# Performance work log

Hardware: AMD Instinct MI355X
Metric: run time of the kernel (lower is better)

Reference implementation:

```python
import jax, jax.numpy as jnp
import numpy as np

KEEP_RATIO = 0.1
FS = 8          # feature_size
BN_EPS = 1e-5


def dct_matrix(N):
    # Orthonormal DCT-II matrix: D[k,n] = s_k * cos(pi*(2n+1)*k/(2N))
    n = jnp.arange(N, dtype=jnp.float32)
    k = n[:, None]
    D = jnp.cos(jnp.pi * (2.0 * n + 1.0) * k / (2.0 * N))
    scale = jnp.full((N, 1), jnp.sqrt(2.0 / N), jnp.float32).at[0, 0].set(jnp.sqrt(1.0 / N))
    return D * scale


def bilinear_resize(x, out_h, out_w):
    # torch F.interpolate bilinear, align_corners=False (half-pixel centers, no antialias)
    def coords(in_size, out):
        src = (jnp.arange(out, dtype=jnp.float32) + 0.5) * (in_size / out) - 0.5
        src = jnp.clip(src, 0.0, in_size - 1.0)
        i0 = jnp.floor(src).astype(jnp.int32)
        i1 = jnp.minimum(i0 + 1, in_size - 1)
        return i0, i1, src - i0.astype(jnp.float32)
    r0, r1, rw = coords(x.shape[2], out_h)
    c0, c1, cw = coords(x.shape[3], out_w)
    x = x[:, :, r0, :] * (1.0 - rw)[:, None] + x[:, :, r1, :] * rw[:, None]
    x = x[:, :, :, c0] * (1.0 - cw) + x[:, :, :, c1] * cw
    return x


def apply_dct(x):
    H, W = x.shape[2], x.shape[3]
    Dh, Dw = dct_matrix(H), dct_matrix(W)
    # 2D DCT-II (ortho): Y = Dh @ X @ Dw^T
    y = jnp.einsum('hi,bcij,wj->bchw', Dh, x, Dw)
    hk, wk = int(H * KEEP_RATIO), int(W * KEEP_RATIO)
    mask = jnp.zeros((H, W), x.dtype).at[:hk, :wk].set(1.0)  # low-pass keep top-left block
    y = y * mask
    # inverse DCT (ortho): X = Dh^T @ Y @ Dw
    x = jnp.einsum('ih,bchw,jw->bcij', Dh, y, Dw)
    return bilinear_resize(x, FS, FS)


def generate_gradient_image(x):
    # scipy convolve2d flips the kernel, but flipped sobel == -sobel and we take abs,
    # so plain correlation with sobel is equivalent. boundary='wrap' -> circular pad.
    sx = jnp.array([[-1, 0, 1], [-2, 0, 2], [-1, 0, 1]], jnp.float32)
    sy = jnp.array([[-1, -2, -1], [0, 0, 0], [1, 2, 1]], jnp.float32)
    kern = jnp.stack([sx, sy])[:, None]  # [2,1,3,3]
    B, C, H, W = x.shape
    xc = x.reshape(B * C, 1, H, W)
    xp = jnp.pad(xc, ((0, 0), (0, 0), (1, 1), (1, 1)), mode='wrap')
    g = jax.lax.conv_general_dilated(xp, kern, (1, 1), 'VALID')  # [B*C,2,H,W]
    grad = jnp.sqrt(g[:, 0] ** 2 + g[:, 1] ** 2).reshape(B, C, H, W)
    return bilinear_resize(grad, FS, FS)


def feature_extractor(x, w, b, gamma, beta):
    y = jax.lax.conv_general_dilated(x, w, (1, 1), ((1, 1), (1, 1)))
    y = y + b[None, :, None, None]
    # BatchNorm (inference: running_mean=0, running_var=1)
    y = y * (gamma / jnp.sqrt(1.0 + BN_EPS))[None, :, None, None] + beta[None, :, None, None]
    y = jax.nn.relu(y)
    # input is already FS x FS, so AdaptiveAvgPool2d((8,8)) is the identity
    return y


def setup_inputs() -> dict:
    key = jax.random.key(0)
    ks = jax.random.split(key, 10)
    B, C, H, W = 128, 3, 256, 256
    return {
        'x': jax.random.normal(ks[0], (B, C, H, W), jnp.float32),
        'conv_dct_w': jax.random.normal(ks[1], (64, 3, 3, 3), jnp.float32) * 0.1,
        'conv_dct_b': jnp.zeros((64,), jnp.float32),
        'bn_dct_g': jnp.ones((64,), jnp.float32),
        'bn_dct_b': jnp.zeros((64,), jnp.float32),
        'conv_grad_w': jax.random.normal(ks[2], (64, 3, 3, 3), jnp.float32) * 0.1,
        'conv_grad_b': jnp.zeros((64,), jnp.float32),
        'bn_grad_g': jnp.ones((64,), jnp.float32),
        'bn_grad_b': jnp.zeros((64,), jnp.float32),
        'fus_w': jax.random.normal(ks[3], (1, 64), jnp.float32) * 0.1,
        'fus_b': jnp.zeros((1,), jnp.float32),
        'cls_w': jax.random.normal(ks[4], (2, 64 * FS * FS), jnp.float32) * 0.02,
        'cls_b': jnp.zeros((2,), jnp.float32),
    }


def reference(x, conv_dct_w, conv_dct_b, bn_dct_g, bn_dct_b,
              conv_grad_w, conv_grad_b, bn_grad_g, bn_grad_b,
              fus_w, fus_b, cls_w, cls_b):
    dct_in = apply_dct(x)                       # [B,3,8,8]
    grad_in = generate_gradient_image(x)        # [B,3,8,8]
    d = feature_extractor(dct_in, conv_dct_w, conv_dct_b, bn_dct_g, bn_dct_b)    # [B,64,8,8]
    g = feature_extractor(grad_in, conv_grad_w, conv_grad_b, bn_grad_g, bn_grad_b)
    # FeatureFusion: weight = sigmoid(fc(avgpool(d+g)))
    s = jnp.mean(d + g, axis=(2, 3))            # [B,64]
    w = jax.nn.sigmoid(s @ fus_w.T + fus_b)     # [B,1]
    w = w[:, :, None, None]
    fused = w * d + (1.0 - w) * g               # [B,64,8,8]
    flat = fused.reshape(fused.shape[0], -1)
    return flat @ cls_w.T + cls_b               # [B,2]
```

## Files before the change

kernel.cpp:

```cpp
#include <hip/hip_runtime.h>
#include <math.h>


__global__ __launch_bounds__(512) void k_main(const float* __restrict__ x,
                                              float* __restrict__ dct_out,
                                              float* __restrict__ grad_out) {
    __shared__ float F[8][25];
    __shared__ float Et[256][8];
    __shared__ float T[8][256];
    __shared__ float PO[8][64];

    const int img = blockIdx.x;
    const float* xi = x + (size_t)img * 65536;
    const int tid = threadIdx.x;
    const float pi_f = 3.14159274101257324f;

    if (tid >= 256) {
        const int t = tid - 256;
        const int s = t & 3, pq = t >> 2;
        const int p = pq >> 3, q = pq & 7;
        const int dr = s >> 1, dc = s & 1;
        const int r = 32 * p + 15 + dr, c = 32 * q + 15 + dc;
        const float* base = xi + (r - 1) * 256 + (c - 1);
        const float a00 = base[0],   a01 = base[1],   a02 = base[2];
        const float a10 = base[256],                  a12 = base[258];
        const float a20 = base[512], a21 = base[513], a22 = base[514];
        const float gx = (a02 - a00) + 2.0f * (a12 - a10) + (a22 - a20);
        const float gy = (a20 - a00) + 2.0f * (a21 - a01) + (a22 - a02);
        float m = sqrtf(gx * gx + gy * gy);
        m += __shfl_xor(m, 1);
        m += __shfl_xor(m, 2);
        if (s == 0) grad_out[img * 64 + pq] = 0.25f * m;
    } else if (tid < 25) {
        const int k = tid;
        const float scale = (k == 0) ? sqrtf(1.0f / 256.0f) : sqrtf(2.0f / 256.0f);
        for (int p = 0; p < 8; ++p) {
            const int n0 = 32 * p + 15;
            const float a0 = (pi_f * (float)(2 * n0 + 1)) * (float)k / 512.0f;
            const float a1 = (pi_f * (float)(2 * n0 + 3)) * (float)k / 512.0f;
            F[p][k] = 0.5f * (cosf(a0) + cosf(a1)) * scale;
        }
    }
    __syncthreads();

    if (tid < 256) {
        const int j = tid;
        float acc[8] = {0.f, 0.f, 0.f, 0.f, 0.f, 0.f, 0.f, 0.f};
        for (int k = 0; k < 25; ++k) {
            const float scale = (k == 0) ? sqrtf(1.0f / 256.0f) : sqrtf(2.0f / 256.0f);
            const float arg = (pi_f * (float)(2 * j + 1)) * (float)k / 512.0f;
            const float Dkj = cosf(arg) * scale;
            #pragma unroll
            for (int p = 0; p < 8; ++p) acc[p] = fmaf(F[p][k], Dkj, acc[p]);
        }
        #pragma unroll
        for (int p = 0; p < 8; ++p) Et[j][p] = acc[p];
    }
    __syncthreads();

    const int w = tid >> 6, l = tid & 63;
    const int cw = w >> 1, ch = w & 1;
    const int col = ch * 128 + 2 * l;

    float acc[8][2];
    #pragma unroll
    for (int p = 0; p < 8; ++p) { acc[p][0] = 0.f; acc[p][1] = 0.f; }

    const float* px = xi + (size_t)(cw * 64) * 256 + col;
    #pragma unroll 4
    for (int i = 0; i < 64; ++i) {
        const float2 v = *(const float2*)px;
        px += 256;
        const int row = cw * 64 + i;
        const float4 ea = *(const float4*)&Et[row][0];
        const float4 eb = *(const float4*)&Et[row][4];
        acc[0][0] = fmaf(ea.x, v.x, acc[0][0]); acc[0][1] = fmaf(ea.x, v.y, acc[0][1]);
        acc[1][0] = fmaf(ea.y, v.x, acc[1][0]); acc[1][1] = fmaf(ea.y, v.y, acc[1][1]);
        acc[2][0] = fmaf(ea.z, v.x, acc[2][0]); acc[2][1] = fmaf(ea.z, v.y, acc[2][1]);
        acc[3][0] = fmaf(ea.w, v.x, acc[3][0]); acc[3][1] = fmaf(ea.w, v.y, acc[3][1]);
        acc[4][0] = fmaf(eb.x, v.x, acc[4][0]); acc[4][1] = fmaf(eb.x, v.y, acc[4][1]);
        acc[5][0] = fmaf(eb.y, v.x, acc[5][0]); acc[5][1] = fmaf(eb.y, v.y, acc[5][1]);
        acc[6][0] = fmaf(eb.z, v.x, acc[6][0]); acc[6][1] = fmaf(eb.z, v.y, acc[6][1]);
        acc[7][0] = fmaf(eb.w, v.x, acc[7][0]); acc[7][1] = fmaf(eb.w, v.y, acc[7][1]);
    }

    for (int r = 0; r < 4; ++r) {
        if (cw == r) {
            if (r == 0) {
                #pragma unroll
                for (int p = 0; p < 8; ++p) {
                    float2 t; t.x = acc[p][0]; t.y = acc[p][1];
                    *(float2*)&T[p][col] = t;
                }
            } else {
                #pragma unroll
                for (int p = 0; p < 8; ++p) {
                    float2 t = *(const float2*)&T[p][col];
                    t.x += acc[p][0]; t.y += acc[p][1];
                    *(float2*)&T[p][col] = t;
                }
            }
        }
        __syncthreads();
    }

    const int pq = tid & 63, seg = tid >> 6;
    const int p = pq >> 3, q = pq & 7;
    float s = 0.0f;
    const int j0 = seg * 32;
    for (int j = j0; j < j0 + 32; ++j) s = fmaf(T[p][j], Et[j][q], s);
    PO[seg][pq] = s;
    __syncthreads();
    if (tid < 64) {
        float r = PO[0][tid] + PO[1][tid] + PO[2][tid] + PO[3][tid] +
                  PO[4][tid] + PO[5][tid] + PO[6][tid] + PO[7][tid];
        dct_out[img * 64 + tid] = r;
    }
}

__global__ __launch_bounds__(256) void k_head(
    const float* __restrict__ dct_in, const float* __restrict__ grad_in,
    const float* __restrict__ wd, const float* __restrict__ bd,
    const float* __restrict__ gd, const float* __restrict__ betad,
    const float* __restrict__ wg, const float* __restrict__ bg,
    const float* __restrict__ gg, const float* __restrict__ betag,
    const float* __restrict__ fus_w, const float* __restrict__ fus_b,
    const float* __restrict__ cls_w, const float* __restrict__ cls_b,
    float* __restrict__ out) {
    __shared__ float ind[3][8][8];
    __shared__ float ing[3][8][8];
    __shared__ float wdl[1728];
    __shared__ float wgl[1728];
    __shared__ float redS[256];
    __shared__ float redF[64];
    __shared__ float fusedS[64][65];
    __shared__ float redW0[4];
    __shared__ float redW1[4];
    __shared__ float wshare;

    const int b = blockIdx.x;
    const int tid = threadIdx.x;
    const int co = tid & 63;
    const int chunk = tid >> 6;

    float* pind = &ind[0][0][0];
    float* ping = &ing[0][0][0];
    for (int i = tid; i < 192; i += 256) {
        pind[i] = dct_in[b * 192 + i];
        ping[i] = grad_in[b * 192 + i];
    }
    for (int i = tid; i < 1728; i += 256) {
        wdl[i] = wd[i];
        wgl[i] = wg[i];
    }
    __syncthreads();

    const float scale_d = gd[co] / sqrtf(1.0f + 1e-5f);
    const float scale_g = gg[co] / sqrtf(1.0f + 1e-5f);
    const float beta_d = betad[co];
    const float beta_g = betag[co];
    const float bias_d = bd[co];
    const float bias_g = bg[co];

    float dreg[16], greg[16];
    float ssum = 0.0f;
    int idx = 0;
    for (int pr = chunk * 2; pr < chunk * 2 + 2; ++pr) {
        for (int qc = 0; qc < 8; ++qc) {
            float sd = bias_d, sg = bias_g;
            for (int ci = 0; ci < 3; ++ci) {
                #pragma unroll
                for (int du = 0; du < 3; ++du) {
                    const int r = pr + du - 1;
                    if (r < 0 || r > 7) continue;
                    #pragma unroll
                    for (int dv = 0; dv < 3; ++dv) {
                        const int c = qc + dv - 1;
                        if (c < 0 || c > 7) continue;
                        const float wv_d = wdl[co * 27 + ci * 9 + du * 3 + dv];
                        const float wv_g = wgl[co * 27 + ci * 9 + du * 3 + dv];
                        sd = fmaf(wv_d, ind[ci][r][c], sd);
                        sg = fmaf(wv_g, ing[ci][r][c], sg);
                    }
                }
            }
            sd = fmaxf(sd * scale_d + beta_d, 0.0f);
            sg = fmaxf(sg * scale_g + beta_g, 0.0f);
            dreg[idx] = sd;
            greg[idx] = sg;
            ssum += sd + sg;
            ++idx;
        }
    }

    redS[tid] = ssum;
    __syncthreads();
    if (tid < 64) {
        const float s =
            (redS[co] + redS[64 + co] + redS[128 + co] + redS[192 + co]) *
            (1.0f / 64.0f);
        redF[co] = s * fus_w[co];
    }
    __syncthreads();
    if (tid < 64) {
        float v = redF[tid];
        #pragma unroll
        for (int off = 1; off < 64; off <<= 1) v += __shfl_xor(v, off);
        if (tid == 0) wshare = 1.0f / (1.0f + expf(-(v + fus_b[0])));
    }
    __syncthreads();
    const float wgt = wshare;

    idx = 0;
    for (int pr = chunk * 2; pr < chunk * 2 + 2; ++pr) {
        for (int qc = 0; qc < 8; ++qc) {
            const float f = wgt * dreg[idx] + (1.0f - wgt) * greg[idx];
            fusedS[co][pr * 8 + qc] = f;
            ++idx;
        }
    }
    __syncthreads();

    const int l = tid & 63, wv = tid >> 6;
    float a0 = 0.0f, a1 = 0.0f;
    #pragma unroll
    for (int k = 0; k < 16; ++k) {
        const int n = tid + 256 * k;
        const float f = fusedS[wv + 4 * k][l];
        a0 = fmaf(f, cls_w[n], a0);
        a1 = fmaf(f, cls_w[4096 + n], a1);
    }
    #pragma unroll
    for (int off = 1; off < 64; off <<= 1) {
        a0 += __shfl_xor(a0, off);
        a1 += __shfl_xor(a1, off);
    }
    if (l == 0) { redW0[wv] = a0; redW1[wv] = a1; }
    __syncthreads();
    if (tid == 0) out[b * 2 + 0] = cls_b[0] + redW0[0] + redW0[1] + redW0[2] + redW0[3];
    if (tid == 1) out[b * 2 + 1] = cls_b[1] + redW1[0] + redW1[1] + redW1[2] + redW1[3];
}

extern "C" void kernel_launch(void* const* d_in, const int* in_sizes, int n_in,
                              void* d_out, int out_size, void* d_ws, size_t ws_size,
                              hipStream_t stream) {
    const float* x     = (const float*)d_in[0];
    const float* wd    = (const float*)d_in[1];
    const float* bd    = (const float*)d_in[2];
    const float* gd    = (const float*)d_in[3];
    const float* betad = (const float*)d_in[4];
    const float* wg    = (const float*)d_in[5];
    const float* bg    = (const float*)d_in[6];
    const float* gg    = (const float*)d_in[7];
    const float* betag = (const float*)d_in[8];
    const float* fusw  = (const float*)d_in[9];
    const float* fusb  = (const float*)d_in[10];
    const float* clsw  = (const float*)d_in[11];
    const float* clsb  = (const float*)d_in[12];
    float* out = (float*)d_out;

    float* ws = (float*)d_ws;
    float* dct_in  = ws;
    float* grad_in = ws + 24576;

    k_main<<<384, 512, 0, stream>>>(x, dct_in, grad_in);
    k_head<<<128, 256, 0, stream>>>(dct_in, grad_in, wd, bd, gd, betad,
                                    wg, bg, gg, betag, fusw, fusb, clsw, clsb,
                                    out);
}
```

Baseline: 189.3 us.

## Split each image's DCT row reduction across two blocks with float4 loads

Each image is now processed by two 256-thread blocks, each covering half of the 256 rows. The two partial 8x8 DCT results are written separately and summed in the head kernel. Each thread now loads a float4 instead of a float2 and keeps 32 accumulators. The aim is more blocks in flight to better saturate memory bandwidth across CUs, at the cost of recomputing the Et basis table in both blocks, more register pressure, and an extra partial-sum pass.

New measurement: 188.2 us. About the same (-0.6%).

```diff
diff --git a/kernel.cpp b/kernel.cpp
--- a/kernel.cpp
+++ b/kernel.cpp
@@ -2,23 +2,25 @@
 #include <math.h>
 
 
-__global__ __launch_bounds__(512) void k_main(const float* __restrict__ x,
-                                              float* __restrict__ dct_out,
+__global__ __launch_bounds__(256) void k_main(const float* __restrict__ x,
+                                              float* __restrict__ dct_part,
                                               float* __restrict__ grad_out) {
     __shared__ float F[8][25];
     __shared__ float Et[256][8];
-    __shared__ float T[8][256];
-    __shared__ float PO[8][64];
-
-    const int img = blockIdx.x;
+    __shared__ float T[8][260];
+    __shared__ float PO[4][64];
+
+    const int bid = blockIdx.x;
+    const int img = bid >> 1, half = bid & 1;
     const float* xi = x + (size_t)img * 65536;
     const int tid = threadIdx.x;
     const float pi_f = 3.14159274101257324f;
 
-    if (tid >= 256) {
-        const int t = tid - 256;
+    if (tid >= 128) {
+        const int t = tid - 128;
         const int s = t & 3, pq = t >> 2;
-        const int p = pq >> 3, q = pq & 7;
+        const int pp = pq >> 3, q = pq & 7;
+        const int p = half * 4 + pp;
         const int dr = s >> 1, dc = s & 1;
         const int r = 32 * p + 15 + dr, c = 32 * q + 15 + dc;
         const float* base = xi + (r - 1) * 256 + (c - 1);
@@ -30,7 +32,7 @@
         float m = sqrtf(gx * gx + gy * gy);
         m += __shfl_xor(m, 1);
         m += __shfl_xor(m, 2);
-        if (s == 0) grad_out[img * 64 + pq] = 0.25f * m;
+        if (s == 0) grad_out[img * 64 + p * 8 + q] = 0.25f * m;
     } else if (tid < 25) {
         const int k = tid;
         const float scale = (k == 0) ? sqrtf(1.0f / 256.0f) : sqrtf(2.0f / 256.0f);
@@ -43,7 +45,7 @@
     }
     __syncthreads();
 
-    if (tid < 256) {
+    {
         const int j = tid;
         float acc[8] = {0.f, 0.f, 0.f, 0.f, 0.f, 0.f, 0.f, 0.f};
         for (int k = 0; k < 25; ++k) {
@@ -59,45 +61,50 @@
     __syncthreads();
 
     const int w = tid >> 6, l = tid & 63;
-    const int cw = w >> 1, ch = w & 1;
-    const int col = ch * 128 + 2 * l;
-
-    float acc[8][2];
+    const int col = 4 * l;
+    const int rbase = half * 128 + w * 32;
+
+    float acc[8][4];
     #pragma unroll
-    for (int p = 0; p < 8; ++p) { acc[p][0] = 0.f; acc[p][1] = 0.f; }
-
-    const float* px = xi + (size_t)(cw * 64) * 256 + col;
+    for (int p = 0; p < 8; ++p)
+        #pragma unroll
+        for (int c = 0; c < 4; ++c) acc[p][c] = 0.f;
+
+    const float* px = xi + (size_t)rbase * 256 + col;
     #pragma unroll 4
-    for (int i = 0; i < 64; ++i) {
-        const float2 v = *(const float2*)px;
+    for (int i = 0; i < 32; ++i) {
+        const float4 v = *(const float4*)px;
         px += 256;
-        const int row = cw * 64 + i;
+        const int row = rbase + i;
         const float4 ea = *(const float4*)&Et[row][0];
         const float4 eb = *(const float4*)&Et[row][4];
-        acc[0][0] = fmaf(ea.x, v.x, acc[0][0]); acc[0][1] = fmaf(ea.x, v.y, acc[0][1]);
-        acc[1][0] = fmaf(ea.y, v.x, acc[1][0]); acc[1][1] = fmaf(ea.y, v.y, acc[1][1]);
-        acc[2][0] = fmaf(ea.z, v.x, acc[2][0]); acc[2][1] = fmaf(ea.z, v.y, acc[2][1]);
-        acc[3][0] = fmaf(ea.w, v.x, acc[3][0]); acc[3][1] = fmaf(ea.w, v.y, acc[3][1]);
-        acc[4][0] = fmaf(eb.x, v.x, acc[4][0]); acc[4][1] = fmaf(eb.x, v.y, acc[4][1]);
-        acc[5][0] = fmaf(eb.y, v.x, acc[5][0]); acc[5][1] = fmaf(eb.y, v.y, acc[5][1]);
-        acc[6][0] = fmaf(eb.z, v.x, acc[6][0]); acc[6][1] = fmaf(eb.z, v.y, acc[6][1]);
-        acc[7][0] = fmaf(eb.w, v.x, acc[7][0]); acc[7][1] = fmaf(eb.w, v.y, acc[7][1]);
+        const float e[8] = {ea.x, ea.y, ea.z, ea.w, eb.x, eb.y, eb.z, eb.w};
+        #pragma unroll
+        for (int p = 0; p < 8; ++p) {
+            acc[p][0] = fmaf(e[p], v.x, acc[p][0]);
+            acc[p][1] = fmaf(e[p], v.y, acc[p][1]);
+            acc[p][2] = fmaf(e[p], v.z, acc[p][2]);
+            acc[p][3] = fmaf(e[p], v.w, acc[p][3]);
+        }
     }
 
     for (int r = 0; r < 4; ++r) {
-        if (cw == r) {
+        if (w == r) {
             if (r == 0) {
                 #pragma unroll
                 for (int p = 0; p < 8; ++p) {
-                    float2 t; t.x = acc[p][0]; t.y = acc[p][1];
-                    *(float2*)&T[p][col] = t;
+                    float4 t;
+                    t.x = acc[p][0]; t.y = acc[p][1];
+                    t.z = acc[p][2]; t.w = acc[p][3];
+                    *(float4*)&T[p][col] = t;
                 }
             } else {
                 #pragma unroll
                 for (int p = 0; p < 8; ++p) {
-                    float2 t = *(const float2*)&T[p][col];
+                    float4 t = *(const float4*)&T[p][col];
                     t.x += acc[p][0]; t.y += acc[p][1];
-                    *(float2*)&T[p][col] = t;
+                    t.z += acc[p][2]; t.w += acc[p][3];
+                    *(float4*)&T[p][col] = t;
                 }
             }
         }
@@ -107,19 +114,18 @@
     const int pq = tid & 63, seg = tid >> 6;
     const int p = pq >> 3, q = pq & 7;
     float s = 0.0f;
-    const int j0 = seg * 32;
-    for (int j = j0; j < j0 + 32; ++j) s = fmaf(T[p][j], Et[j][q], s);
+    const int j0 = seg * 64;
+    for (int j = j0; j < j0 + 64; ++j) s = fmaf(T[p][j], Et[j][q], s);
     PO[seg][pq] = s;
     __syncthreads();
     if (tid < 64) {
-        float r = PO[0][tid] + PO[1][tid] + PO[2][tid] + PO[3][tid] +
-                  PO[4][tid] + PO[5][tid] + PO[6][tid] + PO[7][tid];
-        dct_out[img * 64 + tid] = r;
+        const float r4 = PO[0][tid] + PO[1][tid] + PO[2][tid] + PO[3][tid];
+        dct_part[img * 128 + half * 64 + tid] = r4;
     }
 }
 
 __global__ __launch_bounds__(256) void k_head(
-    const float* __restrict__ dct_in, const float* __restrict__ grad_in,
+    const float* __restrict__ dct_part, const float* __restrict__ grad_in,
     const float* __restrict__ wd, const float* __restrict__ bd,
     const float* __restrict__ gd, const float* __restrict__ betad,
     const float* __restrict__ wg, const float* __restrict__ bg,
@@ -146,7 +152,9 @@
     float* pind = &ind[0][0][0];
     float* ping = &ing[0][0][0];
     for (int i = tid; i < 192; i += 256) {
-        pind[i] = dct_in[b * 192 + i];
+        const int ci = i >> 6, pq = i & 63;
+        const float* dp = dct_part + (size_t)(3 * b + ci) * 128;
+        pind[i] = dp[pq] + dp[64 + pq];
         ping[i] = grad_in[b * 192 + i];
     }
     for (int i = tid; i < 1728; i += 256) {
@@ -260,11 +268,11 @@
     float* out = (float*)d_out;
 
     float* ws = (float*)d_ws;
-    float* dct_in  = ws;
-    float* grad_in = ws + 24576;
-
-    k_main<<<384, 512, 0, stream>>>(x, dct_in, grad_in);
-    k_head<<<128, 256, 0, stream>>>(dct_in, grad_in, wd, bd, gd, betad,
+    float* dct_part = ws;
+    float* grad_in  = ws + 49152;
+
+    k_main<<<768, 256, 0, stream>>>(x, dct_part, grad_in);
+    k_head<<<128, 256, 0, stream>>>(dct_part, grad_in, wd, bd, gd, betad,
                                     wg, bg, gg, betag, fusw, fusb, clsw, clsb,
                                     out);
 }
```
